# Kernel tuning notes

Measured on AMD Instinct MI355X. Metric: run time of the kernel, lower is better.

## Reference

```python
import jax, jax.numpy as jnp
import numpy as np

B, S = 2, 4096
H, D = 8, 64      # num_heads, per-head embed_dim
W = 128           # window (even)
O = 64            # num_outputs per head
ZERO_VALUE = 0.0


def setup_inputs() -> dict:
    key = jax.random.key(0)
    kq, kk, kv, kwq, kwk, kbq, kbk, ko = jax.random.split(key, 8)
    scale = 1.0 / np.sqrt(D)
    return {
        "q": jax.random.normal(kq, (B, S, H * D), dtype=jnp.float32),
        "k": jax.random.normal(kk, (B, S, H * D), dtype=jnp.float32),
        "v": jax.random.normal(kv, (B, S, H * O), dtype=jnp.float32),
        "Wq": jax.random.normal(kwq, (D, D), dtype=jnp.float32) * scale,
        "bq": jax.random.normal(kbq, (D,), dtype=jnp.float32) * 0.02,
        "Wk": jax.random.normal(kwk, (D, D), dtype=jnp.float32) * scale,
        "bk": jax.random.normal(kbk, (D,), dtype=jnp.float32) * 0.02,
        "ocpe": jax.random.normal(ko, (W + 1, H), dtype=jnp.float32) * 0.02,
    }


def reference(q, k, v, Wq, bq, Wk, bk, ocpe):
    b, s, _ = q.shape
    p = W // 2
    assert s % W == 0
    C = s // W  # number of chunks of size `window`

    # split heads + per-head projections (nn.Linear: x @ W.T + b)
    q = q.reshape(b, s, H, D) @ Wq.T + bq
    k = k.reshape(b, s, H, D) @ Wk.T + bk
    v = v.reshape(b, s, H, O)

    # pad seq dim by window//2 on both sides (matches F.pad in source)
    qp = jnp.pad(q, ((0, 0), (p, p), (0, 0), (0, 0)))
    kp = jnp.pad(k, ((0, 0), (p, p), (0, 0), (0, 0)))
    vp = jnp.pad(v, ((0, 0), (p, p), (0, 0), (0, 0)))

    # overlapping chunks of length 2W (chunk_size=W plus 2*p halo)
    starts = jnp.arange(C) * W                 # (C,)
    loc = jnp.arange(2 * W)                    # (2W,)
    idx = starts[:, None] + loc[None, :]       # (C, 2W) indices into padded seq
    qc = qp[:, idx]                            # (B, C, 2W, H, D)
    kc = kp[:, idx]
    vc = vp[:, idx]                            # (B, C, 2W, H, O)

    scores = jnp.einsum('ncxhd,ncyhd->ncxyh', qc, kc)  # (B,C,2W,2W,H)

    diff = loc[None, :] - loc[:, None]         # j - i, (2W, 2W)
    within = jnp.abs(diff) <= p                # (2W, 2W)
    bias = jnp.where(within[:, :, None],
                     ocpe[jnp.clip(p + diff, 0, W)], 0.0)  # (2W,2W,H)
    scores = scores + bias[None, None]

    # boundary mask: global padded position must lie in [p, s+p)
    pos = starts[:, None] + loc[None, :]       # (C, 2W)
    valid = (pos >= p) & (pos < s + p)         # (C, 2W)
    mask = within[None] & valid[:, :, None] & valid[:, None, :]  # (C,2W,2W)

    scores = jnp.where(mask[None, :, :, :, None], scores, ZERO_VALUE)
    attn = jnp.tanh(scores)

    res = jnp.einsum('ncxyh,ncyhd->ncxd', attn, vc)  # (B,C,2W,O)
    out = res[:, :, p:2 * W - p].reshape(b, s, O)     # middle W rows per chunk

    # attn_flat[b,c,i,d,h] = attn[b,c, i+p, i+d, h]
    r = jnp.arange(W)
    rows = r[:, None] + p                      # (W, 1)
    cols = r[:, None] + jnp.arange(W + 1)[None]  # (W, W+1)
    attn_flat = attn[:, :, rows, cols, :]      # (B, C, W, W+1, H)
    attn_flat = attn_flat.reshape(b, s, W + 1, H)
    return attn_flat, out
```

## Files before the change

kernel.cpp:

```cpp
#include <hip/hip_runtime.h>
#include <cstddef>

#define SB 2
#define SS 4096
#define SH 8
#define SD 64
#define SP 64
#define SNO 129
#define TQ 16
#define WN 144
#define NT16 (SS/TQ)
#define SSTR 168

typedef _Float16 f16;
typedef __attribute__((ext_vector_type(8))) _Float16 f16x8;
typedef __attribute__((ext_vector_type(4))) float floatx4;

union f16frag { f16 h[8]; ushort4 u4[2]; f16x8 v; };

__device__ __forceinline__ float fast_tanh(float x) {
  float ax = fabsf(x);
  float e = __expf(2.0f * ax);
  float t = 1.0f - 2.0f / (e + 1.0f);
  return copysignf(t, x);
}

__device__ __forceinline__ void cvt16(const float* __restrict__ src, f16* __restrict__ dst) {
  float4 x0 = *(const float4*)(src);
  float4 x1 = *(const float4*)(src + 4);
  float4 x2 = *(const float4*)(src + 8);
  float4 x3 = *(const float4*)(src + 12);
  f16frag a, c;
  a.h[0]=(f16)x0.x; a.h[1]=(f16)x0.y; a.h[2]=(f16)x0.z; a.h[3]=(f16)x0.w;
  a.h[4]=(f16)x1.x; a.h[5]=(f16)x1.y; a.h[6]=(f16)x1.z; a.h[7]=(f16)x1.w;
  c.h[0]=(f16)x2.x; c.h[1]=(f16)x2.y; c.h[2]=(f16)x2.z; c.h[3]=(f16)x2.w;
  c.h[4]=(f16)x3.x; c.h[5]=(f16)x3.y; c.h[6]=(f16)x3.z; c.h[7]=(f16)x3.w;
  *(ushort4*)(dst)      = a.u4[0];
  *(ushort4*)(dst + 4)  = a.u4[1];
  *(ushort4*)(dst + 8)  = c.u4[0];
  *(ushort4*)(dst + 12) = c.u4[1];
}

__global__ __launch_bounds__(256) void prep_kernel(
    const float* __restrict__ q, const float* __restrict__ k, const float* __restrict__ v,
    const float* __restrict__ Wq, const float* __restrict__ bq,
    const float* __restrict__ Wk, const float* __restrict__ bk,
    f16* __restrict__ Qf, f16* __restrict__ Kf, f16* __restrict__ Vt)
{
  __shared__ f16 sWq[64*72], sWk[64*72], sQr[64*72], sKr[64*72], sVr[64*72];
  __shared__ float sbq[64], sbk[64];

  int t = threadIdx.x;
  int blk = blockIdx.x;
  int x = blk & 7, j = blk >> 3;
  int c = x*8 + (j & 7);
  int h = (j >> 3) & 7;
  int b = j >> 6;
  int s0 = c * 64;

  int dr = t >> 2, e0 = (t & 3) * 16;
  cvt16(Wq + dr*64 + e0, &sWq[dr*72 + e0]);
  cvt16(Wk + dr*64 + e0, &sWk[dr*72 + e0]);
  {
    size_t rbase = ((size_t)(b*SS + s0 + dr)) * (SH*SD) + h*SD + e0;
    cvt16(q + rbase, &sQr[dr*72 + e0]);
    cvt16(k + rbase, &sKr[dr*72 + e0]);
    cvt16(v + rbase, &sVr[dr*72 + e0]);
  }
  if (t < 64) { sbq[t] = bq[t]; sbk[t] = bk[t]; }
  __syncthreads();

  int lane = t & 63, wave = t >> 6;
  int r16 = lane & 15, g = lane >> 4;

  size_t hsbase = (size_t)(b*SH + h) * SS;

  #pragma unroll
  for (int jj = 0; jj < 4; ++jj) {
    int tt = wave + 4*jj;
    int si = tt >> 2, dj = tt & 3;
    floatx4 accq = {0.f,0.f,0.f,0.f}, acck = {0.f,0.f,0.f,0.f};
    #pragma unroll
    for (int e = 0; e < 64; e += 32) {
      f16x8 aq = *(const f16x8*)&sQr[(si*16 + r16)*72 + e + g*8];
      f16x8 ak = *(const f16x8*)&sKr[(si*16 + r16)*72 + e + g*8];
      f16x8 wq8 = *(const f16x8*)&sWq[(dj*16 + r16)*72 + e + g*8];
      f16x8 wk8 = *(const f16x8*)&sWk[(dj*16 + r16)*72 + e + g*8];
      accq = __builtin_amdgcn_mfma_f32_16x16x32_f16(aq, wq8, accq, 0, 0, 0);
      acck = __builtin_amdgcn_mfma_f32_16x16x32_f16(ak, wk8, acck, 0, 0, 0);
    }
    float biasq = sbq[dj*16 + r16];
    float biask = sbk[dj*16 + r16];
    #pragma unroll
    for (int rr = 0; rr < 4; ++rr) {
      int srow = s0 + si*16 + g*4 + rr;
      Qf[(hsbase + srow)*64 + dj*16 + r16] = (f16)(accq[rr] + biasq);
      Kf[(hsbase + srow)*64 + dj*16 + r16] = (f16)(acck[rr] + biask);
    }
  }

  {
    int d = t >> 2, p4 = t & 3, sc0 = p4 * 16;
    f16frag a, c2;
    #pragma unroll
    for (int j2 = 0; j2 < 8; ++j2) a.h[j2] = sVr[(sc0 + j2)*72 + d];
    #pragma unroll
    for (int j2 = 0; j2 < 8; ++j2) c2.h[j2] = sVr[(sc0 + 8 + j2)*72 + d];
    f16* dst = Vt + ((size_t)(b*SH + h)*64 + d)*SS + s0 + sc0;
    *(ushort4*)dst       = a.u4[0];
    *(ushort4*)(dst + 4) = a.u4[1];
    *(ushort4*)(dst + 8) = c2.u4[0];
    *(ushort4*)(dst + 12)= c2.u4[1];
  }
}

__global__ __launch_bounds__(512, 4) void attn_fused(
    const f16* __restrict__ Qf, const f16* __restrict__ Kf, const f16* __restrict__ Vt,
    const float* __restrict__ ocpe, float* __restrict__ af, float* __restrict__ outp)
{
  __shared__ f16 sPriv[SH][TQ*SSTR];
  __shared__ f16 sAF[TQ*SNO*SH];
  __shared__ float sObT[SH*SNO];

  int t = threadIdx.x;
  int lane = t & 63, wave = t >> 6;
  int r16 = lane & 15, g = lane >> 4;

  int blk = blockIdx.x;
  int x = blk & 7, j = blk >> 3;
  int t16 = x*32 + (j & 31);
  int b = j >> 5;
  int t0 = t16 * TQ, yg0 = t0 - SP;

  int h = wave;
  const f16* qb = Qf + ((size_t)(b*SH + h)*SS + t0 + r16)*64;
  f16x8 qa0 = *(const f16x8*)(qb + g*8);
  f16x8 qa1 = *(const f16x8*)(qb + 32 + g*8);

  for (int idx = t; idx < SNO*SH; idx += 512) {
    int o = idx >> 3, h2 = idx & 7;
    sObT[h2*SNO + o] = ocpe[idx];
  }

  f16* priv = &sPriv[wave][0];
  #pragma unroll
  for (int jj = 0; jj < 4; ++jj)
    priv[r16*SSTR + WN + g*4 + jj] = (f16)0.f;

  __syncthreads();

  const float* ob = &sObT[h*SNO];
  const f16* kbase = Kf + ((size_t)(b*SH + h)*SS)*64;
  floatx4 acc2[4] = {{0.f,0.f,0.f,0.f},{0.f,0.f,0.f,0.f},{0.f,0.f,0.f,0.f},{0.f,0.f,0.f,0.f}};

  bool interior = (t16 >= 4) & (t16 <= 250);

  if (interior) {
    const f16* krow = kbase + (size_t)(yg0 + r16) * 64 + g*8;
    #pragma unroll
    for (int yy = 0; yy < 9; ++yy) {
      f16x8 kb0 = *(const f16x8*)(krow + yy*1024);
      f16x8 kb1 = *(const f16x8*)(krow + yy*1024 + 32);
      floatx4 acc = {0.f,0.f,0.f,0.f};
      acc = __builtin_amdgcn_mfma_f32_16x16x32_f16(qa0, kb0, acc, 0, 0, 0);
      acc = __builtin_amdgcn_mfma_f32_16x16x32_f16(qa1, kb1, acc, 0, 0, 0);
      int y = yy*16 + r16;
      #pragma unroll
      for (int rr = 0; rr < 4; ++rr) {
        int i = g*4 + rr;
        int o = y - i;
        bool ook = (o >= 0) & (o <= 2*SP);
        float a = 0.f;
        if (ook) a = fast_tanh(acc[rr] + ob[o]);
        priv[i*SSTR + y] = (f16)a;
        if (ook) sAF[((size_t)i*SNO + o)*SH + h] = (f16)a;
      }
    }
    const f16* vrow = Vt + ((size_t)(b*SH + h)*64 + r16)*SS + yg0 + g*8;
    #pragma unroll
    for (int ks = 0; ks < 5; ++ks) {
      int yb = ks*32 + g*8;
      f16x8 a0 = *(const f16x8*)&priv[r16*SSTR + yb];
      #pragma unroll
      for (int dq = 0; dq < 4; ++dq) {
        f16x8 bv = *(const f16x8*)(vrow + (size_t)(dq*16)*SS + ks*32);
        acc2[dq] = __builtin_amdgcn_mfma_f32_16x16x32_f16(a0, bv, acc2[dq], 0, 0, 0);
      }
    }
  } else {
    #pragma unroll
    for (int yy = 0; yy < 9; ++yy) {
      int y = yy*16 + r16;
      int ygr = yg0 + y;
      int ygc = min(max(ygr, 0), SS-1);
      bool yok = (ygr >= 0) & (ygr < SS);
      const f16* kr = kbase + (size_t)ygc * 64;
      f16x8 kb0 = *(const f16x8*)(kr + g*8);
      f16x8 kb1 = *(const f16x8*)(kr + 32 + g*8);
      floatx4 acc = {0.f,0.f,0.f,0.f};
      acc = __builtin_amdgcn_mfma_f32_16x16x32_f16(qa0, kb0, acc, 0, 0, 0);
      acc = __builtin_amdgcn_mfma_f32_16x16x32_f16(qa1, kb1, acc, 0, 0, 0);
      #pragma unroll
      for (int rr = 0; rr < 4; ++rr) {
        int i = g*4 + rr;
        int o = y - i;
        bool ook = (o >= 0) & (o <= 2*SP);
        float a = 0.f;
        if (yok & ook) a = fast_tanh(acc[rr] + ob[o]);
        priv[i*SSTR + y] = (f16)a;
        if (ook) sAF[((size_t)i*SNO + o)*SH + h] = (f16)a;
      }
    }
    const f16* vb0 = Vt + ((size_t)(b*SH + h)*64 + r16)*SS;
    #pragma unroll
    for (int ks = 0; ks < 5; ++ks) {
      int yb = ks*32 + g*8;
      int ygr = yg0 + yb;
      int ygc = min(max(ygr, 0), SS-8);
      f16x8 a0 = *(const f16x8*)&priv[r16*SSTR + yb];
      #pragma unroll
      for (int dq = 0; dq < 4; ++dq) {
        f16x8 bv = *(const f16x8*)(vb0 + (size_t)(dq*16)*SS + ygc);
        acc2[dq] = __builtin_amdgcn_mfma_f32_16x16x32_f16(a0, bv, acc2[dq], 0, 0, 0);
      }
    }
  }

  {
    float* po = (float*)priv;
    #pragma unroll
    for (int dq = 0; dq < 4; ++dq)
      #pragma unroll
      for (int rr = 0; rr < 4; ++rr)
        po[(g*4 + rr)*64 + dq*16 + r16] = acc2[dq][rr];
  }

  __syncthreads();

  {
    int e2 = t * 2;
    int i = e2 >> 6, d = e2 & 63;
    float sx = 0.f, sy = 0.f;
    #pragma unroll
    for (int h2 = 0; h2 < SH; ++h2) {
      const float* ph = (const float*)&sPriv[h2][0];
      sx += ph[i*64 + d];
      sy += ph[i*64 + d + 1];
    }
    *(float2*)(outp + ((size_t)b*SS + t0 + i)*64 + d) = make_float2(sx, sy);
  }

  {
    float* afb = af + ((size_t)b*SS + t0) * (size_t)(SNO*SH);
    for (int idx = t; idx < TQ*SNO*SH/4; idx += 512) {
      const f16* s = &sAF[idx*4];
      float4 w = make_float4((float)s[0], (float)s[1], (float)s[2], (float)s[3]);
      *(float4*)(afb + idx*4) = w;
    }
  }
}

extern "C" void kernel_launch(void* const* d_in, const int* in_sizes, int n_in,
                              void* d_out, int out_size, void* d_ws, size_t ws_size,
                              hipStream_t stream) {
  const float* q    = (const float*)d_in[0];
  const float* k    = (const float*)d_in[1];
  const float* v    = (const float*)d_in[2];
  const float* Wq   = (const float*)d_in[3];
  const float* bq   = (const float*)d_in[4];
  const float* Wk   = (const float*)d_in[5];
  const float* bk   = (const float*)d_in[6];
  const float* ocpe = (const float*)d_in[7];

  f16* Kf = (f16*)d_ws;
  f16* Vt = Kf + (size_t)SB*SH*SS*SD;
  f16* Qf = Vt + (size_t)SB*SH*SS*SD;

  float* af = (float*)d_out;
  float* op = af + (size_t)SB*SS*SNO*SH;

  prep_kernel<<<SB*SH*64, 256, 0, stream>>>(q, k, v, Wq, bq, Wk, bk, Qf, Kf, Vt);
  attn_fused<<<SB*NT16, 512, 0, stream>>>(Qf, Kf, Vt, ocpe, af, op);
}
```

Measured before the change: 44.59 us.

## Transpose score MFMA, drop separate attn_flat buffer, read band from private tiles

Swaps the MFMA operands so each lane holds four consecutive key columns of one query row, which lets the tanh results be packed and written to the per-head score tile with a single 8-byte store. The separate sAF shared buffer and its scattered per-element stores are removed. The attn_flat output is now gathered directly from the diagonal band of each head's private tile, and the per-head partial outputs go to a padded dedicated float buffer. The fast tanh uses a hardware reciprocal instead of a divide. The aim is fewer shared-memory stores, fewer bank conflicts and less LDS footprint, in exchange for a strided gather across heads in the output phase.

```diff
diff --git a/kernel.cpp b/kernel.cpp
--- a/kernel.cpp
+++ b/kernel.cpp
@@ -11,17 +11,20 @@
 #define WN 144
 #define NT16 (SS/TQ)
 #define SSTR 168
+#define PRIV (TQ*SSTR + 8)
+#define OSTR 68
 
 typedef _Float16 f16;
 typedef __attribute__((ext_vector_type(8))) _Float16 f16x8;
 typedef __attribute__((ext_vector_type(4))) float floatx4;
 
 union f16frag { f16 h[8]; ushort4 u4[2]; f16x8 v; };
+union pack4 { f16 h[4]; ushort4 u; };
 
 __device__ __forceinline__ float fast_tanh(float x) {
   float ax = fabsf(x);
   float e = __expf(2.0f * ax);
-  float t = 1.0f - 2.0f / (e + 1.0f);
+  float t = 1.0f - 2.0f * __builtin_amdgcn_rcpf(e + 1.0f);
   return copysignf(t, x);
 }
 
@@ -72,7 +75,6 @@
 
   int lane = t & 63, wave = t >> 6;
   int r16 = lane & 15, g = lane >> 4;
-
   size_t hsbase = (size_t)(b*SH + h) * SS;
 
   #pragma unroll
@@ -98,7 +100,6 @@
       Kf[(hsbase + srow)*64 + dj*16 + r16] = (f16)(acck[rr] + biask);
     }
   }
-
   {
     int d = t >> 2, p4 = t & 3, sc0 = p4 * 16;
     f16frag a, c2;
@@ -118,8 +119,8 @@
     const f16* __restrict__ Qf, const f16* __restrict__ Kf, const f16* __restrict__ Vt,
     const float* __restrict__ ocpe, float* __restrict__ af, float* __restrict__ outp)
 {
-  __shared__ f16 sPriv[SH][TQ*SSTR];
-  __shared__ f16 sAF[TQ*SNO*SH];
+  __shared__ f16 sPriv[SH*PRIV];
+  __shared__ float sOutP[SH*TQ*OSTR];
   __shared__ float sObT[SH*SNO];
 
   int t = threadIdx.x;
@@ -141,8 +142,7 @@
     int o = idx >> 3, h2 = idx & 7;
     sObT[h2*SNO + o] = ocpe[idx];
   }
-
-  f16* priv = &sPriv[wave][0];
+  f16* priv = &sPriv[h*PRIV];
   #pragma unroll
   for (int jj = 0; jj < 4; ++jj)
     priv[r16*SSTR + WN + g*4 + jj] = (f16)0.f;
@@ -162,19 +162,19 @@
       f16x8 kb0 = *(const f16x8*)(krow + yy*1024);
       f16x8 kb1 = *(const f16x8*)(krow + yy*1024 + 32);
       floatx4 acc = {0.f,0.f,0.f,0.f};
-      acc = __builtin_amdgcn_mfma_f32_16x16x32_f16(qa0, kb0, acc, 0, 0, 0);
-      acc = __builtin_amdgcn_mfma_f32_16x16x32_f16(qa1, kb1, acc, 0, 0, 0);
-      int y = yy*16 + r16;
+      acc = __builtin_amdgcn_mfma_f32_16x16x32_f16(kb0, qa0, acc, 0, 0, 0);
+      acc = __builtin_amdgcn_mfma_f32_16x16x32_f16(kb1, qa1, acc, 0, 0, 0);
+      int y0 = yy*16 + g*4;
+      pack4 pk;
       #pragma unroll
       for (int rr = 0; rr < 4; ++rr) {
-        int i = g*4 + rr;
-        int o = y - i;
+        int o = y0 + rr - r16;
         bool ook = (o >= 0) & (o <= 2*SP);
         float a = 0.f;
         if (ook) a = fast_tanh(acc[rr] + ob[o]);
-        priv[i*SSTR + y] = (f16)a;
-        if (ook) sAF[((size_t)i*SNO + o)*SH + h] = (f16)a;
-      }
+        pk.h[rr] = (f16)a;
+      }
+      *(ushort4*)&priv[r16*SSTR + y0] = pk.u;
     }
     const f16* vrow = Vt + ((size_t)(b*SH + h)*64 + r16)*SS + yg0 + g*8;
     #pragma unroll
@@ -190,33 +190,33 @@
   } else {
     #pragma unroll
     for (int yy = 0; yy < 9; ++yy) {
-      int y = yy*16 + r16;
-      int ygr = yg0 + y;
-      int ygc = min(max(ygr, 0), SS-1);
-      bool yok = (ygr >= 0) & (ygr < SS);
-      const f16* kr = kbase + (size_t)ygc * 64;
+      int ldr = yg0 + yy*16 + r16;
+      int ldc = min(max(ldr, 0), SS-1);
+      const f16* kr = kbase + (size_t)ldc * 64;
       f16x8 kb0 = *(const f16x8*)(kr + g*8);
       f16x8 kb1 = *(const f16x8*)(kr + 32 + g*8);
       floatx4 acc = {0.f,0.f,0.f,0.f};
-      acc = __builtin_amdgcn_mfma_f32_16x16x32_f16(qa0, kb0, acc, 0, 0, 0);
-      acc = __builtin_amdgcn_mfma_f32_16x16x32_f16(qa1, kb1, acc, 0, 0, 0);
+      acc = __builtin_amdgcn_mfma_f32_16x16x32_f16(kb0, qa0, acc, 0, 0, 0);
+      acc = __builtin_amdgcn_mfma_f32_16x16x32_f16(kb1, qa1, acc, 0, 0, 0);
+      int y0 = yy*16 + g*4;
+      pack4 pk;
       #pragma unroll
       for (int rr = 0; rr < 4; ++rr) {
-        int i = g*4 + rr;
-        int o = y - i;
-        bool ook = (o >= 0) & (o <= 2*SP);
+        int y = y0 + rr;
+        int ygr = yg0 + y;
+        int o = y - r16;
+        bool ok = (ygr >= 0) & (ygr < SS) & (o >= 0) & (o <= 2*SP);
         float a = 0.f;
-        if (yok & ook) a = fast_tanh(acc[rr] + ob[o]);
-        priv[i*SSTR + y] = (f16)a;
-        if (ook) sAF[((size_t)i*SNO + o)*SH + h] = (f16)a;
-      }
+        if (ok) a = fast_tanh(acc[rr] + ob[o]);
+        pk.h[rr] = (f16)a;
+      }
+      *(ushort4*)&priv[r16*SSTR + y0] = pk.u;
     }
     const f16* vb0 = Vt + ((size_t)(b*SH + h)*64 + r16)*SS;
     #pragma unroll
     for (int ks = 0; ks < 5; ++ks) {
       int yb = ks*32 + g*8;
-      int ygr = yg0 + yb;
-      int ygc = min(max(ygr, 0), SS-8);
+      int ygc = min(max(yg0 + yb, 0), SS-8);
       f16x8 a0 = *(const f16x8*)&priv[r16*SSTR + yb];
       #pragma unroll
       for (int dq = 0; dq < 4; ++dq) {
@@ -227,12 +227,12 @@
   }
 
   {
-    float* po = (float*)priv;
+    float* po = &sOutP[h*TQ*OSTR];
     #pragma unroll
     for (int dq = 0; dq < 4; ++dq)
       #pragma unroll
       for (int rr = 0; rr < 4; ++rr)
-        po[(g*4 + rr)*64 + dq*16 + r16] = acc2[dq][rr];
+        po[(g*4 + rr)*OSTR + dq*16 + r16] = acc2[dq][rr];
   }
 
   __syncthreads();
@@ -243,19 +243,29 @@
     float sx = 0.f, sy = 0.f;
     #pragma unroll
     for (int h2 = 0; h2 < SH; ++h2) {
-      const float* ph = (const float*)&sPriv[h2][0];
-      sx += ph[i*64 + d];
-      sy += ph[i*64 + d + 1];
+      const float* ph = &sOutP[h2*TQ*OSTR];
+      sx += ph[i*OSTR + d];
+      sy += ph[i*OSTR + d + 1];
     }
     *(float2*)(outp + ((size_t)b*SS + t0 + i)*64 + d) = make_float2(sx, sy);
   }
 
   {
-    float* afb = af + ((size_t)b*SS + t0) * (size_t)(SNO*SH);
-    for (int idx = t; idx < TQ*SNO*SH/4; idx += 512) {
-      const f16* s = &sAF[idx*4];
-      float4 w = make_float4((float)s[0], (float)s[1], (float)s[2], (float)s[3]);
-      *(float4*)(afb + idx*4) = w;
+    int i = t >> 5, o0 = t & 31;
+    int rb = i*SSTR + i;
+    float* afb = af + (((size_t)b*SS + t0 + i)*SNO)*SH;
+    #pragma unroll
+    for (int jj = 0; jj < 5; ++jj) {
+      int o = o0 + 32*jj;
+      if (o < SNO) {
+        float v0[8];
+        #pragma unroll
+        for (int hh = 0; hh < 8; ++hh)
+          v0[hh] = (float)sPriv[hh*PRIV + rb + o];
+        float* dst = afb + (size_t)o*SH;
+        *(float4*)dst       = make_float4(v0[0], v0[1], v0[2], v0[3]);
+        *(float4*)(dst + 4) = make_float4(v0[4], v0[5], v0[6], v0[7]);
+      }
     }
   }
 }
```

Result: slower. 48.99 us (+9.9%).

## Replace shared-memory head reduction with atomics and write attn_flat directly

Applied to the files above, without the earlier changes.

Removes the shared-memory staging buffer for attn_flat and writes each tanh value straight to global memory as a strided scalar store. It also drops the cross-head reduction through shared memory and the trailing __syncthreads, accumulating per-head outputs with global atomicAdd into an output buffer that prep_kernel zeroes. fast_tanh becomes a branch-free form using a hardware reciprocal. The cost is uncoalesced 4-byte stores with a stride of 8 floats, plus roughly 8x more atomic traffic on the output, in exchange for lower LDS use and fewer barriers.

```diff
diff --git a/kernel.cpp b/kernel.cpp
--- a/kernel.cpp
+++ b/kernel.cpp
@@ -19,10 +19,8 @@
 union f16frag { f16 h[8]; ushort4 u4[2]; f16x8 v; };
 
 __device__ __forceinline__ float fast_tanh(float x) {
-  float ax = fabsf(x);
-  float e = __expf(2.0f * ax);
-  float t = 1.0f - 2.0f / (e + 1.0f);
-  return copysignf(t, x);
+  float e = __expf(2.0f * x);
+  return 1.0f - 2.0f * __builtin_amdgcn_rcpf(e + 1.0f);
 }
 
 __device__ __forceinline__ void cvt16(const float* __restrict__ src, f16* __restrict__ dst) {
@@ -45,7 +43,8 @@
     const float* __restrict__ q, const float* __restrict__ k, const float* __restrict__ v,
     const float* __restrict__ Wq, const float* __restrict__ bq,
     const float* __restrict__ Wk, const float* __restrict__ bk,
-    f16* __restrict__ Qf, f16* __restrict__ Kf, f16* __restrict__ Vt)
+    f16* __restrict__ Qf, f16* __restrict__ Kf, f16* __restrict__ Vt,
+    float* __restrict__ outp)
 {
   __shared__ f16 sWq[64*72], sWk[64*72], sQr[64*72], sKr[64*72], sVr[64*72];
   __shared__ float sbq[64], sbk[64];
@@ -57,6 +56,8 @@
   int h = (j >> 3) & 7;
   int b = j >> 6;
   int s0 = c * 64;
+
+  *(float2*)(outp + (size_t)blk * 512 + t * 2) = make_float2(0.f, 0.f);
 
   int dr = t >> 2, e0 = (t & 3) * 16;
   cvt16(Wq + dr*64 + e0, &sWq[dr*72 + e0]);
@@ -72,7 +73,6 @@
 
   int lane = t & 63, wave = t >> 6;
   int r16 = lane & 15, g = lane >> 4;
-
   size_t hsbase = (size_t)(b*SH + h) * SS;
 
   #pragma unroll
@@ -98,7 +98,6 @@
       Kf[(hsbase + srow)*64 + dj*16 + r16] = (f16)(acck[rr] + biask);
     }
   }
-
   {
     int d = t >> 2, p4 = t & 3, sc0 = p4 * 16;
     f16frag a, c2;
@@ -119,7 +118,6 @@
     const float* __restrict__ ocpe, float* __restrict__ af, float* __restrict__ outp)
 {
   __shared__ f16 sPriv[SH][TQ*SSTR];
-  __shared__ f16 sAF[TQ*SNO*SH];
   __shared__ float sObT[SH*SNO];
 
   int t = threadIdx.x;
@@ -141,7 +139,6 @@
     int o = idx >> 3, h2 = idx & 7;
     sObT[h2*SNO + o] = ocpe[idx];
   }
-
   f16* priv = &sPriv[wave][0];
   #pragma unroll
   for (int jj = 0; jj < 4; ++jj)
@@ -151,6 +148,7 @@
 
   const float* ob = &sObT[h*SNO];
   const f16* kbase = Kf + ((size_t)(b*SH + h)*SS)*64;
+  float* afh = af + ((size_t)(b*SS + t0) * SNO) * SH + h;
   floatx4 acc2[4] = {{0.f,0.f,0.f,0.f},{0.f,0.f,0.f,0.f},{0.f,0.f,0.f,0.f},{0.f,0.f,0.f,0.f}};
 
   bool interior = (t16 >= 4) & (t16 <= 250);
@@ -170,10 +168,10 @@
         int i = g*4 + rr;
         int o = y - i;
         bool ook = (o >= 0) & (o <= 2*SP);
-        float a = 0.f;
-        if (ook) a = fast_tanh(acc[rr] + ob[o]);
-        priv[i*SSTR + y] = (f16)a;
-        if (ook) sAF[((size_t)i*SNO + o)*SH + h] = (f16)a;
+        f16 ah = (f16)0.f;
+        if (ook) ah = (f16)fast_tanh(acc[rr] + ob[o]);
+        priv[i*SSTR + y] = ah;
+        if (ook) afh[(i*SNO + o) * SH] = (float)ah;
       }
     }
     const f16* vrow = Vt + ((size_t)(b*SH + h)*64 + r16)*SS + yg0 + g*8;
@@ -205,10 +203,10 @@
         int i = g*4 + rr;
         int o = y - i;
         bool ook = (o >= 0) & (o <= 2*SP);
-        float a = 0.f;
-        if (yok & ook) a = fast_tanh(acc[rr] + ob[o]);
-        priv[i*SSTR + y] = (f16)a;
-        if (ook) sAF[((size_t)i*SNO + o)*SH + h] = (f16)a;
+        f16 ah = (f16)0.f;
+        if (yok & ook) ah = (f16)fast_tanh(acc[rr] + ob[o]);
+        priv[i*SSTR + y] = ah;
+        if (ook) afh[(i*SNO + o) * SH] = (float)ah;
       }
     }
     const f16* vb0 = Vt + ((size_t)(b*SH + h)*64 + r16)*SS;
@@ -226,38 +224,11 @@
     }
   }
 
-  {
-    float* po = (float*)priv;
-    #pragma unroll
-    for (int dq = 0; dq < 4; ++dq)
-      #pragma unroll
-      for (int rr = 0; rr < 4; ++rr)
-        po[(g*4 + rr)*64 + dq*16 + r16] = acc2[dq][rr];
-  }
-
-  __syncthreads();
-
-  {
-    int e2 = t * 2;
-    int i = e2 >> 6, d = e2 & 63;
-    float sx = 0.f, sy = 0.f;
-    #pragma unroll
-    for (int h2 = 0; h2 < SH; ++h2) {
-      const float* ph = (const float*)&sPriv[h2][0];
-      sx += ph[i*64 + d];
-      sy += ph[i*64 + d + 1];
-    }
-    *(float2*)(outp + ((size_t)b*SS + t0 + i)*64 + d) = make_float2(sx, sy);
-  }
-
-  {
-    float* afb = af + ((size_t)b*SS + t0) * (size_t)(SNO*SH);
-    for (int idx = t; idx < TQ*SNO*SH/4; idx += 512) {
-      const f16* s = &sAF[idx*4];
-      float4 w = make_float4((float)s[0], (float)s[1], (float)s[2], (float)s[3]);
-      *(float4*)(afb + idx*4) = w;
-    }
-  }
+  #pragma unroll
+  for (int dq = 0; dq < 4; ++dq)
+    #pragma unroll
+    for (int rr = 0; rr < 4; ++rr)
+      atomicAdd(outp + ((size_t)b*SS + t0 + g*4 + rr)*64 + dq*16 + r16, acc2[dq][rr]);
 }
 
 extern "C" void kernel_launch(void* const* d_in, const int* in_sizes, int n_in,
@@ -279,6 +250,6 @@
   float* af = (float*)d_out;
   float* op = af + (size_t)SB*SS*SNO*SH;
 
-  prep_kernel<<<SB*SH*64, 256, 0, stream>>>(q, k, v, Wq, bq, Wk, bk, Qf, Kf, Vt);
+  prep_kernel<<<SB*SH*64, 256, 0, stream>>>(q, k, v, Wq, bq, Wk, bk, Qf, Kf, Vt, op);
   attn_fused<<<SB*NT16, 512, 0, stream>>>(Qf, Kf, Vt, ocpe, af, op);
 }
```

Result: slower. 59.44 us (+33.3%).
